# Optimization experiments

Hardware: AMD Instinct MI355X
Metric: run time of the kernel (lower is better)

## Reference

```python
import jax, jax.numpy as jnp
import numpy as np

EMB = 256
HID = 256
NH = 8
HD = HID // NH  # 32
EPS = 1e-5


def _wn(v, g):
    # torch weight_norm(dim=0): per-output-row normalization of v
    return g[:, None] * v / jnp.linalg.norm(v, axis=1, keepdims=True)


def _ln(x, gamma, beta):
    mu = jnp.mean(x, axis=-1, keepdims=True)
    var = jnp.mean((x - mu) ** 2, axis=-1, keepdims=True)
    return (x - mu) * jax.lax.rsqrt(var + EPS) * gamma + beta


def _rope(x):
    # x: [B', S, H, D]; torchtune-style rotary embedding, base 10000
    S, D = x.shape[1], x.shape[3]
    freqs = 1.0 / (10000.0 ** (jnp.arange(0, D, 2, dtype=jnp.float32) / D))  # [D/2]
    ang = jnp.arange(S, dtype=jnp.float32)[:, None] * freqs[None, :]          # [S, D/2]
    cos = jnp.cos(ang)[None, :, None, :]
    sin = jnp.sin(ang)[None, :, None, :]
    xr = x.reshape(*x.shape[:-1], D // 2, 2)
    x0, x1 = xr[..., 0], xr[..., 1]
    out = jnp.stack([x0 * cos - x1 * sin, x1 * cos + x0 * sin], axis=-1)
    return out.reshape(x.shape)


def setup_inputs() -> dict:
    key = jax.random.key(0)
    ks = jax.random.split(key, 12)
    s = lambda shp: 0.02
    return {
        "z": jax.random.normal(ks[0], (2, 32, 512, EMB), dtype=jnp.float32),
        "ln1_g": jnp.ones((EMB,), jnp.float32),
        "ln1_b": jnp.zeros((EMB,), jnp.float32),
        "proj_v": jax.random.normal(ks[1], (3 * HID, EMB), jnp.float32) * 0.02,
        "proj_g": jnp.ones((3 * HID,), jnp.float32),
        "proj_b": jnp.zeros((3 * HID,), jnp.float32),
        "ff_v": jax.random.normal(ks[2], (EMB, HID), jnp.float32) * 0.02,
        "ff_g": jnp.ones((EMB,), jnp.float32),
        "ff_b": jnp.zeros((EMB,), jnp.float32),
        "ln2_g": jnp.ones((EMB,), jnp.float32),
        "ln2_b": jnp.zeros((EMB,), jnp.float32),
        "w1_v": jax.random.normal(ks[3], (EMB, EMB), jnp.float32) * 0.02,
        "w1_g": jnp.ones((EMB,), jnp.float32),
        "w1_b": jnp.zeros((EMB,), jnp.float32),
        "w2_v": jax.random.normal(ks[4], (EMB, EMB), jnp.float32) * 0.02,
        "w2_g": jnp.ones((EMB,), jnp.float32),
        "w2_b": jnp.zeros((EMB,), jnp.float32),
    }


def reference(z, ln1_g, ln1_b, proj_v, proj_g, proj_b, ff_v, ff_g, ff_b,
              ln2_g, ln2_b, w1_v, w1_g, w1_b, w2_v, w2_g, w2_b):
    B, U, A, E = z.shape
    BU = B * U
    Wqkv = _wn(proj_v, proj_g)   # [3H, E]
    Wo = _wn(ff_v, ff_g)         # [E, H]
    # ---- RoPE attention block ----
    z_ = _ln(z, ln1_g, ln1_b).reshape(BU, A, E)
    qkv = z_ @ Wqkv.T + proj_b                       # [BU, A, 3H]
    qkv = qkv.reshape(BU, A, NH, 3 * HD)
    q, k, v = jnp.split(qkv, 3, axis=-1)             # each [BU, A, NH, HD]
    q = _rope(q)
    k = _rope(k)
    qh = q.transpose(0, 2, 1, 3)                     # [BU, NH, A, HD]
    kh = k.transpose(0, 2, 1, 3)
    vh = v.transpose(0, 2, 1, 3)
    scores = jnp.einsum('bhqd,bhkd->bhqk', qh, kh) / jnp.sqrt(jnp.float32(HD))
    attn = jax.nn.softmax(scores, axis=-1)
    out = jnp.einsum('bhqk,bhkd->bhqd', attn, vh)    # [BU, NH, A, HD]
    out = out.transpose(0, 2, 1, 3).reshape(BU, A, HID)
    out = out @ Wo.T + ff_b
    z = z + out.reshape(B, U, A, E)
    # ---- NormFF block ----
    W1 = _wn(w1_v, w1_g)
    W2 = _wn(w2_v, w2_g)
    h = _ln(z, ln2_g, ln2_b)
    h = jax.nn.gelu(h @ W1.T + w1_b, approximate=False)
    h = h @ W2.T + w2_b
    return z + h
```

## Files before the change

### kernel.cpp

```cpp
#include <hip/hip_runtime.h>
#include <cmath>

#define EMB 256
#define NHEAD 8
#define HD 32
#define A_LEN 512
#define TOK 32768

typedef __bf16 bf16_t;
typedef __bf16 bf16x8 __attribute__((ext_vector_type(8)));
typedef __bf16 bf16x4 __attribute__((ext_vector_type(4)));
typedef float floatx4 __attribute__((ext_vector_type(4)));

#define MFMA16(a, b, c) __builtin_amdgcn_mfma_f32_16x16x32_bf16((a), (b), (c), 0, 0, 0)

__global__ __launch_bounds__(64) void setup_kernel(
    const float* __restrict__ proj_v, const float* __restrict__ proj_g,
    const float* __restrict__ ff_v, const float* __restrict__ ff_g,
    const float* __restrict__ w1_v, const float* __restrict__ w1_g,
    const float* __restrict__ w2_v, const float* __restrict__ w2_g,
    bf16_t* __restrict__ Wall, float* __restrict__ ctab,
    float* __restrict__ stab) {
    int b = blockIdx.x;
    int lane = threadIdx.x;
    if (b < 1536) {
        const float* v; const float* g; int r;
        if (b < 768)       { v = proj_v; g = proj_g; r = b; }
        else if (b < 1024) { v = ff_v;   g = ff_g;   r = b - 768; }
        else if (b < 1280) { v = w1_v;   g = w1_g;   r = b - 1024; }
        else               { v = w2_v;   g = w2_g;   r = b - 1280; }
        const floatx4* vr = (const floatx4*)(v + (size_t)r * 256);
        floatx4 x = vr[lane];
        float ss = x[0] * x[0] + x[1] * x[1] + x[2] * x[2] + x[3] * x[3];
#pragma unroll
        for (int off = 32; off >= 1; off >>= 1) ss += __shfl_xor(ss, off);
        float sc = g[r] * rsqrtf(ss);
        bf16x4 o;
        o[0] = (bf16_t)(x[0] * sc); o[1] = (bf16_t)(x[1] * sc);
        o[2] = (bf16_t)(x[2] * sc); o[3] = (bf16_t)(x[3] * sc);
        ((bf16x4*)(Wall + (size_t)b * 256))[lane] = o;
    } else {
        int idx = (b - 1536) * 64 + lane;
        int a = idx >> 4, i = idx & 15;
        float freq = expf(-(float)(2 * i) * 0.2878231366242558f);
        float ang = (float)a * freq;
        ctab[idx] = cosf(ang);
        stab[idx] = sinf(ang);
    }
}

__global__ __launch_bounds__(256, 2) void qkv_kernel(
    const float* __restrict__ z, const float* __restrict__ ln_g,
    const float* __restrict__ ln_b, const bf16_t* __restrict__ W,
    const float* __restrict__ pb, const float* __restrict__ ctab,
    const float* __restrict__ stab, bf16_t* __restrict__ qbf,
    bf16_t* __restrict__ kbf, bf16_t* __restrict__ vtb) {
    __shared__ bf16_t xns[64 * 264];
    __shared__ bf16_t vls[256 * 72];
    int tid = threadIdx.x;
    int t0 = blockIdx.x * 64;

#pragma unroll
    for (int it = 0; it < 4; ++it) {
        int row = it * 16 + (tid >> 4);
        int sub = tid & 15;
        const floatx4* zr = (const floatx4*)(z + (size_t)(t0 + row) * 256 + sub * 16);
        floatx4 v0 = zr[0], v1 = zr[1], v2 = zr[2], v3 = zr[3];
        float vals[16];
        ((floatx4*)vals)[0] = v0; ((floatx4*)vals)[1] = v1;
        ((floatx4*)vals)[2] = v2; ((floatx4*)vals)[3] = v3;
        float s = 0.f, q2 = 0.f;
#pragma unroll
        for (int i = 0; i < 16; ++i) { s += vals[i]; q2 += vals[i] * vals[i]; }
#pragma unroll
        for (int off = 8; off >= 1; off >>= 1) {
            s += __shfl_xor(s, off);
            q2 += __shfl_xor(q2, off);
        }
        float mu = s * (1.f / 256.f);
        float inv = rsqrtf(q2 * (1.f / 256.f) - mu * mu + 1e-5f);
        int cb = sub * 16;
        bf16x8 o0, o1;
#pragma unroll
        for (int i = 0; i < 8; ++i)
            o0[i] = (bf16_t)((vals[i] - mu) * inv * ln_g[cb + i] + ln_b[cb + i]);
#pragma unroll
        for (int i = 0; i < 8; ++i)
            o1[i] = (bf16_t)((vals[8 + i] - mu) * inv * ln_g[cb + 8 + i] + ln_b[cb + 8 + i]);
        *(bf16x8*)&xns[row * 264 + cb] = o0;
        *(bf16x8*)&xns[row * 264 + cb + 8] = o1;
    }
    __syncthreads();

    int wv = tid >> 6, lane = tid & 63, quad = lane >> 4, lidx = lane & 15;

    bf16x8 afr[4][8];
#pragma unroll
    for (int mt = 0; mt < 4; ++mt)
#pragma unroll
        for (int kc = 0; kc < 8; ++kc)
            afr[mt][kc] = *(const bf16x8*)&xns[(mt * 16 + lidx) * 264 + kc * 32 + quad * 8];

#pragma unroll 1
    for (int nt = 0; nt < 12; ++nt) {
        int nbase = wv * 192 + nt * 16;
        int n = nbase + lidx;
        bf16x8 bfr[8];
#pragma unroll
        for (int kc = 0; kc < 8; ++kc)
            bfr[kc] = *(const bf16x8*)&W[(size_t)n * 256 + kc * 32 + quad * 8];
        floatx4 acc[4];
#pragma unroll
        for (int mt = 0; mt < 4; ++mt) acc[mt] = (floatx4){0.f, 0.f, 0.f, 0.f};
#pragma unroll
        for (int kc = 0; kc < 8; ++kc)
#pragma unroll
            for (int mt = 0; mt < 4; ++mt)
                acc[mt] = MFMA16(afr[mt][kc], bfr[kc], acc[mt]);

        float bias = pb[n];
        int htile = nbase / 96;
        int rem = nbase % 96;
        int sec = rem >> 5;
        int d = (rem & 31) + lidx;
#pragma unroll
        for (int mt = 0; mt < 4; ++mt) {
#pragma unroll
            for (int r = 0; r < 4; ++r) {
                int tok = t0 + mt * 16 + quad * 4 + r;
                int a = tok & 511;
                int bu = tok >> 9;
                float val = acc[mt][r] + bias;
                if (sec == 2) {
                    int a_loc = mt * 16 + quad * 4 + r;
                    vls[(htile * 32 + d) * 72 + a_loc] = (bf16_t)val;
                } else {
                    size_t addr = ((size_t)((bu * 8 + htile) * 512 + a)) * 32 + d;
                    float part = __shfl_xor(val, 1);
                    float cs = ctab[a * 16 + (d >> 1)];
                    float sn = stab[a * 16 + (d >> 1)];
                    float res = ((d & 1) == 0) ? (val * cs - part * sn)
                                               : (val * cs + part * sn);
                    if (sec == 0)
                        qbf[addr] = (bf16_t)(res * 0.17677669529663687f);
                    else
                        kbf[addr] = (bf16_t)res;
                }
            }
        }
    }
    __syncthreads();
    {
        int bu = t0 >> 9, a0 = t0 & 511;
        size_t gbase = ((size_t)(bu * 256 + tid)) * 512 + a0;
#pragma unroll
        for (int j = 0; j < 8; ++j)
            *(bf16x8*)&vtb[gbase + j * 8] = *(const bf16x8*)&vls[tid * 72 + j * 8];
    }
}

__global__ __launch_bounds__(512, 4) void attn_kernel(
    const bf16_t* __restrict__ qbf, const bf16_t* __restrict__ kbf,
    const bf16_t* __restrict__ vtb, bf16_t* __restrict__ ob) {
    __shared__ bf16_t Kls[512 * 32];
    __shared__ bf16_t Vt[32 * 512];
    __shared__ bf16_t Pls[8 * 16 * 64];
    int tid = threadIdx.x;
    int wv = tid >> 6, lane = tid & 63, quad = lane >> 4, lidx = lane & 15;
    int bh = blockIdx.x;
    int bu = bh >> 3, h = bh & 7;
    size_t hb = (size_t)bh * (A_LEN * HD);

#pragma unroll
    for (int i = 0; i < 4; ++i) {
        int c = tid + i * 512;
        int key = c >> 2, blk = c & 3;
        bf16x8 kv = *(const bf16x8*)&kbf[hb + (size_t)c * 8];
        *(bf16x8*)&Kls[key * 32 + ((blk ^ (key & 3)) << 3)] = kv;
        int vrow = c >> 6, vblk = c & 63;
        bf16x8 vv = *(const bf16x8*)&vtb[hb + (size_t)c * 8];
        *(bf16x8*)&Vt[vrow * 512 + ((vblk ^ (vrow & 7)) << 3)] = vv;
    }
    __syncthreads();

    int pbase = wv * (16 * 64);
    const floatx4 cm8 = (floatx4){-8.f, -8.f, -8.f, -8.f};
    const floatx4 zero4 = (floatx4){0.f, 0.f, 0.f, 0.f};

#pragma unroll 1
    for (int mt = 0; mt < 4; ++mt) {
        int q0 = wv * 64 + mt * 16;
        bf16x8 qfrag = *(const bf16x8*)&qbf[hb + (size_t)(q0 + lidx) * 32 + quad * 8];
        float l_[4] = {0.f, 0.f, 0.f, 0.f};
        floatx4 Oacc[2];
        Oacc[0] = zero4; Oacc[1] = zero4;

#pragma unroll 1
        for (int kc = 0; kc < 8; ++kc) {
            floatx4 sc[4];
#pragma unroll
            for (int t = 0; t < 4; ++t) {
                bf16x8 kf = *(const bf16x8*)&Kls[(kc * 64 + t * 16 + lidx) * 32 +
                                                 ((quad ^ (lidx & 3)) << 3)];
                sc[t] = MFMA16(qfrag, kf, cm8);
            }
            float p[4][4];
#pragma unroll
            for (int t = 0; t < 4; ++t)
#pragma unroll
                for (int r = 0; r < 4; ++r) p[t][r] = __expf(sc[t][r]);
#pragma unroll
            for (int t = 0; t < 4; ++t)
#pragma unroll
                for (int r = 0; r < 4; ++r) {
                    int row = quad * 4 + r;
                    int pc = (t * 16 + lidx) ^ ((row & 7) << 3);
                    Pls[pbase + row * 64 + pc] = (bf16_t)p[t][r];
                }
#pragma unroll
            for (int r = 0; r < 4; ++r) {
                float s = (p[0][r] + p[1][r]) + (p[2][r] + p[3][r]);
#pragma unroll
                for (int off = 8; off >= 1; off >>= 1) s += __shfl_xor(s, off);
                l_[r] += s;
            }
#pragma unroll
            for (int ks = 0; ks < 2; ++ks) {
                bf16x8 pf = *(const bf16x8*)&Pls[pbase + lidx * 64 +
                                                 (((ks * 4 + quad) ^ (lidx & 7)) << 3)];
#pragma unroll
                for (int nt = 0; nt < 2; ++nt) {
                    int vrow = nt * 16 + lidx;
                    bf16x8 vf = *(const bf16x8*)&Vt[vrow * 512 +
                        ((kc * 8 + ((ks * 4 + quad) ^ (lidx & 7))) << 3)];
                    Oacc[nt] = MFMA16(pf, vf, Oacc[nt]);
                }
            }
        }
#pragma unroll
        for (int nt = 0; nt < 2; ++nt)
#pragma unroll
            for (int r = 0; r < 4; ++r) {
                int tok = bu * 512 + q0 + quad * 4 + r;
                ob[(size_t)tok * 256 + h * 32 + nt * 16 + lidx] =
                    (bf16_t)(Oacc[nt][r] / l_[r]);
            }
    }
}

__global__ __launch_bounds__(256, 2) void tail_kernel(
    const bf16_t* __restrict__ X, const bf16_t* __restrict__ Wo,
    const float* __restrict__ obias, const float* __restrict__ zin,
    const float* __restrict__ ln_g, const float* __restrict__ ln_b,
    const bf16_t* __restrict__ W1, const float* __restrict__ b1,
    const bf16_t* __restrict__ W2, const float* __restrict__ b2,
    float* __restrict__ outp) {
    __shared__ bf16_t xns[64 * 264];
    __shared__ bf16_t hs[64 * 264];
    __shared__ float red[64 * 8];
    __shared__ float mi[64 * 2];
    int tid = threadIdx.x;
    int t0 = blockIdx.x * 64;
    int wv = tid >> 6, lane = tid & 63, quad = lane >> 4, lidx = lane & 15;

    bf16x8 afr[4][8];
#pragma unroll
    for (int mt = 0; mt < 4; ++mt)
#pragma unroll
        for (int kc = 0; kc < 8; ++kc)
            afr[mt][kc] = *(const bf16x8*)&X[(size_t)(t0 + mt * 16 + lidx) * 256 + kc * 32 + quad * 8];

    float r1[4][4][4];
#pragma unroll 1
    for (int nt = 0; nt < 4; ++nt) {
        int n = wv * 64 + nt * 16 + lidx;
        bf16x8 bfr[8];
#pragma unroll
        for (int kc = 0; kc < 8; ++kc)
            bfr[kc] = *(const bf16x8*)&Wo[(size_t)n * 256 + kc * 32 + quad * 8];
        floatx4 acc[4];
#pragma unroll
        for (int mt = 0; mt < 4; ++mt) acc[mt] = (floatx4){0.f, 0.f, 0.f, 0.f};
#pragma unroll
        for (int kc = 0; kc < 8; ++kc)
#pragma unroll
            for (int mt = 0; mt < 4; ++mt)
                acc[mt] = MFMA16(afr[mt][kc], bfr[kc], acc[mt]);
        float b = obias[n];
#pragma unroll
        for (int mt = 0; mt < 4; ++mt)
#pragma unroll
            for (int r = 0; r < 4; ++r) {
                size_t o = (size_t)(t0 + mt * 16 + quad * 4 + r) * 256 + n;
                r1[nt][mt][r] = zin[o] + acc[mt][r] + b;
            }
    }

#pragma unroll
    for (int mt = 0; mt < 4; ++mt)
#pragma unroll
        for (int r = 0; r < 4; ++r) {
            float s = 0.f, ss = 0.f;
#pragma unroll
            for (int nt = 0; nt < 4; ++nt) {
                float v = r1[nt][mt][r];
                s += v; ss += v * v;
            }
#pragma unroll
            for (int off = 8; off >= 1; off >>= 1) {
                s += __shfl_xor(s, off);
                ss += __shfl_xor(ss, off);
            }
            if (lidx == 0) {
                int row = mt * 16 + quad * 4 + r;
                red[row * 8 + wv * 2] = s;
                red[row * 8 + wv * 2 + 1] = ss;
            }
        }
    __syncthreads();
    if (tid < 64) {
        float s = 0.f, ss = 0.f;
#pragma unroll
        for (int w = 0; w < 4; ++w) {
            s += red[tid * 8 + w * 2];
            ss += red[tid * 8 + w * 2 + 1];
        }
        float mu = s * (1.f / 256.f);
        mi[tid * 2] = mu;
        mi[tid * 2 + 1] = rsqrtf(ss * (1.f / 256.f) - mu * mu + 1e-5f);
    }
    __syncthreads();

    float gv[4], bv[4];
#pragma unroll
    for (int nt = 0; nt < 4; ++nt) {
        int n = wv * 64 + nt * 16 + lidx;
        gv[nt] = ln_g[n]; bv[nt] = ln_b[n];
    }
#pragma unroll
    for (int mt = 0; mt < 4; ++mt)
#pragma unroll
        for (int r = 0; r < 4; ++r) {
            int row = mt * 16 + quad * 4 + r;
            float mu = mi[row * 2], inv = mi[row * 2 + 1];
#pragma unroll
            for (int nt = 0; nt < 4; ++nt) {
                int n = wv * 64 + nt * 16 + lidx;
                xns[row * 264 + n] = (bf16_t)((r1[nt][mt][r] - mu) * inv * gv[nt] + bv[nt]);
            }
        }
    __syncthreads();

#pragma unroll
    for (int mt = 0; mt < 4; ++mt)
#pragma unroll
        for (int kc = 0; kc < 8; ++kc)
            afr[mt][kc] = *(const bf16x8*)&xns[(mt * 16 + lidx) * 264 + kc * 32 + quad * 8];
#pragma unroll 1
    for (int nt = 0; nt < 4; ++nt) {
        int n = wv * 64 + nt * 16 + lidx;
        bf16x8 bfr[8];
#pragma unroll
        for (int kc = 0; kc < 8; ++kc)
            bfr[kc] = *(const bf16x8*)&W1[(size_t)n * 256 + kc * 32 + quad * 8];
        floatx4 acc[4];
#pragma unroll
        for (int mt = 0; mt < 4; ++mt) acc[mt] = (floatx4){0.f, 0.f, 0.f, 0.f};
#pragma unroll
        for (int kc = 0; kc < 8; ++kc)
#pragma unroll
            for (int mt = 0; mt < 4; ++mt)
                acc[mt] = MFMA16(afr[mt][kc], bfr[kc], acc[mt]);
        float b = b1[n];
#pragma unroll
        for (int mt = 0; mt < 4; ++mt)
#pragma unroll
            for (int r = 0; r < 4; ++r) {
                float x = acc[mt][r] + b;
                float gel = 0.5f * x * (1.f + erff(x * 0.7071067811865476f));
                hs[(mt * 16 + quad * 4 + r) * 264 + n] = (bf16_t)gel;
            }
    }
    __syncthreads();

#pragma unroll
    for (int mt = 0; mt < 4; ++mt)
#pragma unroll
        for (int kc = 0; kc < 8; ++kc)
            afr[mt][kc] = *(const bf16x8*)&hs[(mt * 16 + lidx) * 264 + kc * 32 + quad * 8];
#pragma unroll 1
    for (int nt = 0; nt < 4; ++nt) {
        int n = wv * 64 + nt * 16 + lidx;
        bf16x8 bfr[8];
#pragma unroll
        for (int kc = 0; kc < 8; ++kc)
            bfr[kc] = *(const bf16x8*)&W2[(size_t)n * 256 + kc * 32 + quad * 8];
        floatx4 acc[4];
#pragma unroll
        for (int mt = 0; mt < 4; ++mt) acc[mt] = (floatx4){0.f, 0.f, 0.f, 0.f};
#pragma unroll
        for (int kc = 0; kc < 8; ++kc)
#pragma unroll
            for (int mt = 0; mt < 4; ++mt)
                acc[mt] = MFMA16(afr[mt][kc], bfr[kc], acc[mt]);
        float b = b2[n];
#pragma unroll
        for (int mt = 0; mt < 4; ++mt)
#pragma unroll
            for (int r = 0; r < 4; ++r) {
                size_t o = (size_t)(t0 + mt * 16 + quad * 4 + r) * 256 + n;
                outp[o] = r1[nt][mt][r] + acc[mt][r] + b;
            }
    }
}

extern "C" void kernel_launch(void* const* d_in, const int* in_sizes, int n_in,
                              void* d_out, int out_size, void* d_ws, size_t ws_size,
                              hipStream_t stream) {
    const float* z      = (const float*)d_in[0];
    const float* ln1_g  = (const float*)d_in[1];
    const float* ln1_b  = (const float*)d_in[2];
    const float* proj_v = (const float*)d_in[3];
    const float* proj_g = (const float*)d_in[4];
    const float* proj_b = (const float*)d_in[5];
    const float* ff_v   = (const float*)d_in[6];
    const float* ff_g   = (const float*)d_in[7];
    const float* ff_b   = (const float*)d_in[8];
    const float* ln2_g  = (const float*)d_in[9];
    const float* ln2_b  = (const float*)d_in[10];
    const float* w1_v   = (const float*)d_in[11];
    const float* w1_g   = (const float*)d_in[12];
    const float* w1_b   = (const float*)d_in[13];
    const float* w2_v   = (const float*)d_in[14];
    const float* w2_g   = (const float*)d_in[15];
    const float* w2_b   = (const float*)d_in[16];
    float* out = (float*)d_out;

    char* p = (char*)d_ws;
    bf16_t* Wall = (bf16_t*)p; p += (size_t)1536 * 256 * 2;
    float* ctab  = (float*)p;  p += 8192 * 4;
    float* stab  = (float*)p;  p += 8192 * 4;
    bf16_t* qbf  = (bf16_t*)p; p += (size_t)TOK * 256 * 2;
    bf16_t* kbf  = (bf16_t*)p; p += (size_t)TOK * 256 * 2;
    bf16_t* vtb  = (bf16_t*)p; p += (size_t)TOK * 256 * 2;
    bf16_t* abuf = (bf16_t*)p; p += (size_t)TOK * 256 * 2;

    const bf16_t* Wqkv = Wall;
    const bf16_t* Wo   = Wall + (size_t)768 * 256;
    const bf16_t* W1   = Wall + (size_t)1024 * 256;
    const bf16_t* W2   = Wall + (size_t)1280 * 256;

    setup_kernel<<<1664, 64, 0, stream>>>(proj_v, proj_g, ff_v, ff_g,
                                          w1_v, w1_g, w2_v, w2_g,
                                          Wall, ctab, stab);
    qkv_kernel<<<TOK / 64, 256, 0, stream>>>(z, ln1_g, ln1_b, Wqkv, proj_b,
                                             ctab, stab, qbf, kbf, vtb);
    attn_kernel<<<64 * 8, 512, 0, stream>>>(qbf, kbf, vtb, abuf);
    tail_kernel<<<TOK / 64, 256, 0, stream>>>(abuf, Wo, ff_b, z, ln2_g, ln2_b,
                                              W1, w1_b, W2, w2_b, out);
}
```

Before: 289.0 us.

## Halve token tiles in QKV and tail kernels to raise occupancy

Shrinks the token tile in the QKV and tail GEMM kernels from 64 to 32 rows and raises launch bounds to 4 blocks per CU. The inner loops now stream A fragments from LDS per k-chunk instead of holding 32 register fragments, which cuts register and LDS pressure. The tail kernel reuses one LDS buffer across its stages and stages the final output through LDS so it can be written as coalesced float4 stores. Each block now reads every weight row for half as many tokens, so weight traffic per token doubles, and extra barriers are added.

```diff
diff --git a/kernel.cpp b/kernel.cpp
--- a/kernel.cpp
+++ b/kernel.cpp
@@ -49,19 +49,19 @@
     }
 }
 
-__global__ __launch_bounds__(256, 2) void qkv_kernel(
+__global__ __launch_bounds__(256, 4) void qkv_kernel(
     const float* __restrict__ z, const float* __restrict__ ln_g,
     const float* __restrict__ ln_b, const bf16_t* __restrict__ W,
     const float* __restrict__ pb, const float* __restrict__ ctab,
     const float* __restrict__ stab, bf16_t* __restrict__ qbf,
     bf16_t* __restrict__ kbf, bf16_t* __restrict__ vtb) {
-    __shared__ bf16_t xns[64 * 264];
-    __shared__ bf16_t vls[256 * 72];
+    __shared__ bf16_t xns[32 * 264];
+    __shared__ bf16_t vls[256 * 40];
     int tid = threadIdx.x;
-    int t0 = blockIdx.x * 64;
-
-#pragma unroll
-    for (int it = 0; it < 4; ++it) {
+    int t0 = blockIdx.x * 32;
+
+#pragma unroll
+    for (int it = 0; it < 2; ++it) {
         int row = it * 16 + (tid >> 4);
         int sub = tid & 15;
         const floatx4* zr = (const floatx4*)(z + (size_t)(t0 + row) * 256 + sub * 16);
@@ -94,68 +94,69 @@
 
     int wv = tid >> 6, lane = tid & 63, quad = lane >> 4, lidx = lane & 15;
 
-    bf16x8 afr[4][8];
-#pragma unroll
-    for (int mt = 0; mt < 4; ++mt)
-#pragma unroll
-        for (int kc = 0; kc < 8; ++kc)
-            afr[mt][kc] = *(const bf16x8*)&xns[(mt * 16 + lidx) * 264 + kc * 32 + quad * 8];
-
 #pragma unroll 1
-    for (int nt = 0; nt < 12; ++nt) {
-        int nbase = wv * 192 + nt * 16;
-        int n = nbase + lidx;
-        bf16x8 bfr[8];
-#pragma unroll
-        for (int kc = 0; kc < 8; ++kc)
-            bfr[kc] = *(const bf16x8*)&W[(size_t)n * 256 + kc * 32 + quad * 8];
-        floatx4 acc[4];
-#pragma unroll
-        for (int mt = 0; mt < 4; ++mt) acc[mt] = (floatx4){0.f, 0.f, 0.f, 0.f};
-#pragma unroll
-        for (int kc = 0; kc < 8; ++kc)
-#pragma unroll
-            for (int mt = 0; mt < 4; ++mt)
-                acc[mt] = MFMA16(afr[mt][kc], bfr[kc], acc[mt]);
-
-        float bias = pb[n];
-        int htile = nbase / 96;
-        int rem = nbase % 96;
-        int sec = rem >> 5;
-        int d = (rem & 31) + lidx;
-#pragma unroll
-        for (int mt = 0; mt < 4; ++mt) {
-#pragma unroll
-            for (int r = 0; r < 4; ++r) {
-                int tok = t0 + mt * 16 + quad * 4 + r;
-                int a = tok & 511;
-                int bu = tok >> 9;
-                float val = acc[mt][r] + bias;
-                if (sec == 2) {
+    for (int g = 0; g < 3; ++g) {
+        floatx4 acc[4][2];
+#pragma unroll
+        for (int i = 0; i < 4; ++i) {
+            acc[i][0] = (floatx4){0.f, 0.f, 0.f, 0.f};
+            acc[i][1] = (floatx4){0.f, 0.f, 0.f, 0.f};
+        }
+#pragma unroll 2
+        for (int kc = 0; kc < 8; ++kc) {
+            bf16x8 a0 = *(const bf16x8*)&xns[lidx * 264 + kc * 32 + quad * 8];
+            bf16x8 a1 = *(const bf16x8*)&xns[(16 + lidx) * 264 + kc * 32 + quad * 8];
+#pragma unroll
+            for (int ntl = 0; ntl < 4; ++ntl) {
+                int n = wv * 192 + (g * 4 + ntl) * 16 + lidx;
+                bf16x8 bfr = *(const bf16x8*)&W[(size_t)n * 256 + kc * 32 + quad * 8];
+                acc[ntl][0] = MFMA16(a0, bfr, acc[ntl][0]);
+                acc[ntl][1] = MFMA16(a1, bfr, acc[ntl][1]);
+            }
+        }
+#pragma unroll
+        for (int ntl = 0; ntl < 4; ++ntl) {
+            int nbase = wv * 192 + (g * 4 + ntl) * 16;
+            int n = nbase + lidx;
+            float bias = pb[n];
+            int htile = nbase / 96;
+            int rem = nbase % 96;
+            int sec = rem >> 5;
+            int d = (rem & 31) + lidx;
+#pragma unroll
+            for (int mt = 0; mt < 2; ++mt) {
+#pragma unroll
+                for (int r = 0; r < 4; ++r) {
                     int a_loc = mt * 16 + quad * 4 + r;
-                    vls[(htile * 32 + d) * 72 + a_loc] = (bf16_t)val;
-                } else {
-                    size_t addr = ((size_t)((bu * 8 + htile) * 512 + a)) * 32 + d;
-                    float part = __shfl_xor(val, 1);
-                    float cs = ctab[a * 16 + (d >> 1)];
-                    float sn = stab[a * 16 + (d >> 1)];
-                    float res = ((d & 1) == 0) ? (val * cs - part * sn)
-                                               : (val * cs + part * sn);
-                    if (sec == 0)
-                        qbf[addr] = (bf16_t)(res * 0.17677669529663687f);
-                    else
-                        kbf[addr] = (bf16_t)res;
-                }
-            }
-        }
-    }
-    __syncthreads();
-    {
-        int bu = t0 >> 9, a0 = t0 & 511;
-        size_t gbase = ((size_t)(bu * 256 + tid)) * 512 + a0;
-#pragma unroll
-        for (int j = 0; j < 8; ++j)
-            *(bf16x8*)&vtb[gbase + j * 8] = *(const bf16x8*)&vls[tid * 72 + j * 8];
+                    int tok = t0 + a_loc;
+                    int a = tok & 511;
+                    int bu = tok >> 9;
+                    float val = acc[ntl][mt][r] + bias;
+                    if (sec == 2) {
+                        vls[(htile * 32 + d) * 40 + a_loc] = (bf16_t)val;
+                    } else {
+                        size_t addr = ((size_t)((bu * 8 + htile) * 512 + a)) * 32 + d;
+                        float part = __shfl_xor(val, 1);
+                        float cs = ctab[a * 16 + (d >> 1)];
+                        float sn = stab[a * 16 + (d >> 1)];
+                        float res = ((d & 1) == 0) ? (val * cs - part * sn)
+                                                   : (val * cs + part * sn);
+                        if (sec == 0)
+                            qbf[addr] = (bf16_t)(res * 0.17677669529663687f);
+                        else
+                            kbf[addr] = (bf16_t)res;
+                    }
+                }
+            }
+        }
+    }
+    __syncthreads();
+    {
+        int bu = t0 >> 9, ac0 = t0 & 511;
+        size_t gbase = ((size_t)(bu * 256 + tid)) * 512 + ac0;
+#pragma unroll
+        for (int j = 0; j < 4; ++j)
+            *(bf16x8*)&vtb[gbase + j * 8] = *(const bf16x8*)&vls[tid * 40 + j * 8];
     }
 }
 
@@ -248,56 +249,66 @@
     }
 }
 
-__global__ __launch_bounds__(256, 2) void tail_kernel(
+__global__ __launch_bounds__(256, 4) void tail_kernel(
     const bf16_t* __restrict__ X, const bf16_t* __restrict__ Wo,
     const float* __restrict__ obias, const float* __restrict__ zin,
     const float* __restrict__ ln_g, const float* __restrict__ ln_b,
     const bf16_t* __restrict__ W1, const float* __restrict__ b1,
     const bf16_t* __restrict__ W2, const float* __restrict__ b2,
     float* __restrict__ outp) {
-    __shared__ bf16_t xns[64 * 264];
-    __shared__ bf16_t hs[64 * 264];
-    __shared__ float red[64 * 8];
-    __shared__ float mi[64 * 2];
+    __shared__ float fbuf[32 * 264];
+    __shared__ float red[32 * 8];
+    __shared__ float mi[32 * 2];
+    bf16_t* xbuf = (bf16_t*)fbuf;
     int tid = threadIdx.x;
-    int t0 = blockIdx.x * 64;
+    int t0 = blockIdx.x * 32;
     int wv = tid >> 6, lane = tid & 63, quad = lane >> 4, lidx = lane & 15;
 
-    bf16x8 afr[4][8];
-#pragma unroll
-    for (int mt = 0; mt < 4; ++mt)
-#pragma unroll
-        for (int kc = 0; kc < 8; ++kc)
-            afr[mt][kc] = *(const bf16x8*)&X[(size_t)(t0 + mt * 16 + lidx) * 256 + kc * 32 + quad * 8];
-
-    float r1[4][4][4];
-#pragma unroll 1
-    for (int nt = 0; nt < 4; ++nt) {
-        int n = wv * 64 + nt * 16 + lidx;
-        bf16x8 bfr[8];
-#pragma unroll
-        for (int kc = 0; kc < 8; ++kc)
-            bfr[kc] = *(const bf16x8*)&Wo[(size_t)n * 256 + kc * 32 + quad * 8];
-        floatx4 acc[4];
-#pragma unroll
-        for (int mt = 0; mt < 4; ++mt) acc[mt] = (floatx4){0.f, 0.f, 0.f, 0.f};
-#pragma unroll
-        for (int kc = 0; kc < 8; ++kc)
-#pragma unroll
-            for (int mt = 0; mt < 4; ++mt)
-                acc[mt] = MFMA16(afr[mt][kc], bfr[kc], acc[mt]);
-        float b = obias[n];
-#pragma unroll
-        for (int mt = 0; mt < 4; ++mt)
-#pragma unroll
-            for (int r = 0; r < 4; ++r) {
-                size_t o = (size_t)(t0 + mt * 16 + quad * 4 + r) * 256 + n;
-                r1[nt][mt][r] = zin[o] + acc[mt][r] + b;
-            }
-    }
-
-#pragma unroll
-    for (int mt = 0; mt < 4; ++mt)
+    {
+        int row = tid >> 3;
+        int c0 = (tid & 7) * 32;
+        const bf16x8* src = (const bf16x8*)&X[(size_t)(t0 + row) * 256 + c0];
+        bf16x8* dst = (bf16x8*)&xbuf[row * 264 + c0];
+        dst[0] = src[0]; dst[1] = src[1]; dst[2] = src[2]; dst[3] = src[3];
+    }
+    __syncthreads();
+
+    float r1[4][2][4];
+    {
+        floatx4 acc[4][2];
+#pragma unroll
+        for (int i = 0; i < 4; ++i) {
+            acc[i][0] = (floatx4){0.f, 0.f, 0.f, 0.f};
+            acc[i][1] = (floatx4){0.f, 0.f, 0.f, 0.f};
+        }
+#pragma unroll 2
+        for (int kc = 0; kc < 8; ++kc) {
+            bf16x8 a0 = *(const bf16x8*)&xbuf[lidx * 264 + kc * 32 + quad * 8];
+            bf16x8 a1 = *(const bf16x8*)&xbuf[(16 + lidx) * 264 + kc * 32 + quad * 8];
+#pragma unroll
+            for (int nt = 0; nt < 4; ++nt) {
+                int n = wv * 64 + nt * 16 + lidx;
+                bf16x8 bfr = *(const bf16x8*)&Wo[(size_t)n * 256 + kc * 32 + quad * 8];
+                acc[nt][0] = MFMA16(a0, bfr, acc[nt][0]);
+                acc[nt][1] = MFMA16(a1, bfr, acc[nt][1]);
+            }
+        }
+#pragma unroll
+        for (int nt = 0; nt < 4; ++nt) {
+            int n = wv * 64 + nt * 16 + lidx;
+            float b = obias[n];
+#pragma unroll
+            for (int mt = 0; mt < 2; ++mt)
+#pragma unroll
+                for (int r = 0; r < 4; ++r) {
+                    size_t o = (size_t)(t0 + mt * 16 + quad * 4 + r) * 256 + n;
+                    r1[nt][mt][r] = zin[o] + acc[nt][mt][r] + b;
+                }
+        }
+    }
+
+#pragma unroll
+    for (int mt = 0; mt < 2; ++mt)
 #pragma unroll
         for (int r = 0; r < 4; ++r) {
             float s = 0.f, ss = 0.f;
@@ -318,7 +329,7 @@
             }
         }
     __syncthreads();
-    if (tid < 64) {
+    if (tid < 32) {
         float s = 0.f, ss = 0.f;
 #pragma unroll
         for (int w = 0; w < 4; ++w) {
@@ -331,86 +342,106 @@
     }
     __syncthreads();
 
-    float gv[4], bv[4];
-#pragma unroll
-    for (int nt = 0; nt < 4; ++nt) {
-        int n = wv * 64 + nt * 16 + lidx;
-        gv[nt] = ln_g[n]; bv[nt] = ln_b[n];
-    }
-#pragma unroll
-    for (int mt = 0; mt < 4; ++mt)
-#pragma unroll
-        for (int r = 0; r < 4; ++r) {
-            int row = mt * 16 + quad * 4 + r;
-            float mu = mi[row * 2], inv = mi[row * 2 + 1];
+    {
+        float gv[4], bv[4];
+#pragma unroll
+        for (int nt = 0; nt < 4; ++nt) {
+            int n = wv * 64 + nt * 16 + lidx;
+            gv[nt] = ln_g[n]; bv[nt] = ln_b[n];
+        }
+#pragma unroll
+        for (int mt = 0; mt < 2; ++mt)
+#pragma unroll
+            for (int r = 0; r < 4; ++r) {
+                int row = mt * 16 + quad * 4 + r;
+                float mu = mi[row * 2], inv = mi[row * 2 + 1];
+#pragma unroll
+                for (int nt = 0; nt < 4; ++nt) {
+                    int n = wv * 64 + nt * 16 + lidx;
+                    xbuf[row * 264 + n] =
+                        (bf16_t)((r1[nt][mt][r] - mu) * inv * gv[nt] + bv[nt]);
+                }
+            }
+    }
+    __syncthreads();
+
+    {
+        floatx4 acc[4][2];
+#pragma unroll
+        for (int i = 0; i < 4; ++i) {
+            acc[i][0] = (floatx4){0.f, 0.f, 0.f, 0.f};
+            acc[i][1] = (floatx4){0.f, 0.f, 0.f, 0.f};
+        }
+#pragma unroll 2
+        for (int kc = 0; kc < 8; ++kc) {
+            bf16x8 a0 = *(const bf16x8*)&xbuf[lidx * 264 + kc * 32 + quad * 8];
+            bf16x8 a1 = *(const bf16x8*)&xbuf[(16 + lidx) * 264 + kc * 32 + quad * 8];
 #pragma unroll
             for (int nt = 0; nt < 4; ++nt) {
                 int n = wv * 64 + nt * 16 + lidx;
-                xns[row * 264 + n] = (bf16_t)((r1[nt][mt][r] - mu) * inv * gv[nt] + bv[nt]);
-            }
-        }
-    __syncthreads();
-
-#pragma unroll
-    for (int mt = 0; mt < 4; ++mt)
-#pragma unroll
-        for (int kc = 0; kc < 8; ++kc)
-            afr[mt][kc] = *(const bf16x8*)&xns[(mt * 16 + lidx) * 264 + kc * 32 + quad * 8];
-#pragma unroll 1
-    for (int nt = 0; nt < 4; ++nt) {
-        int n = wv * 64 + nt * 16 + lidx;
-        bf16x8 bfr[8];
-#pragma unroll
-        for (int kc = 0; kc < 8; ++kc)
-            bfr[kc] = *(const bf16x8*)&W1[(size_t)n * 256 + kc * 32 + quad * 8];
-        floatx4 acc[4];
-#pragma unroll
-        for (int mt = 0; mt < 4; ++mt) acc[mt] = (floatx4){0.f, 0.f, 0.f, 0.f};
-#pragma unroll
-        for (int kc = 0; kc < 8; ++kc)
-#pragma unroll
-            for (int mt = 0; mt < 4; ++mt)
-                acc[mt] = MFMA16(afr[mt][kc], bfr[kc], acc[mt]);
-        float b = b1[n];
-#pragma unroll
-        for (int mt = 0; mt < 4; ++mt)
-#pragma unroll
-            for (int r = 0; r < 4; ++r) {
-                float x = acc[mt][r] + b;
-                float gel = 0.5f * x * (1.f + erff(x * 0.7071067811865476f));
-                hs[(mt * 16 + quad * 4 + r) * 264 + n] = (bf16_t)gel;
-            }
-    }
-    __syncthreads();
-
-#pragma unroll
-    for (int mt = 0; mt < 4; ++mt)
-#pragma unroll
-        for (int kc = 0; kc < 8; ++kc)
-            afr[mt][kc] = *(const bf16x8*)&hs[(mt * 16 + lidx) * 264 + kc * 32 + quad * 8];
-#pragma unroll 1
-    for (int nt = 0; nt < 4; ++nt) {
-        int n = wv * 64 + nt * 16 + lidx;
-        bf16x8 bfr[8];
-#pragma unroll
-        for (int kc = 0; kc < 8; ++kc)
-            bfr[kc] = *(const bf16x8*)&W2[(size_t)n * 256 + kc * 32 + quad * 8];
-        floatx4 acc[4];
-#pragma unroll
-        for (int mt = 0; mt < 4; ++mt) acc[mt] = (floatx4){0.f, 0.f, 0.f, 0.f};
-#pragma unroll
-        for (int kc = 0; kc < 8; ++kc)
-#pragma unroll
-            for (int mt = 0; mt < 4; ++mt)
-                acc[mt] = MFMA16(afr[mt][kc], bfr[kc], acc[mt]);
-        float b = b2[n];
-#pragma unroll
-        for (int mt = 0; mt < 4; ++mt)
-#pragma unroll
-            for (int r = 0; r < 4; ++r) {
-                size_t o = (size_t)(t0 + mt * 16 + quad * 4 + r) * 256 + n;
-                outp[o] = r1[nt][mt][r] + acc[mt][r] + b;
-            }
+                bf16x8 bfr = *(const bf16x8*)&W1[(size_t)n * 256 + kc * 32 + quad * 8];
+                acc[nt][0] = MFMA16(a0, bfr, acc[nt][0]);
+                acc[nt][1] = MFMA16(a1, bfr, acc[nt][1]);
+            }
+        }
+        __syncthreads();
+#pragma unroll
+        for (int nt = 0; nt < 4; ++nt) {
+            int n = wv * 64 + nt * 16 + lidx;
+            float b = b1[n];
+#pragma unroll
+            for (int mt = 0; mt < 2; ++mt)
+#pragma unroll
+                for (int r = 0; r < 4; ++r) {
+                    float x = acc[nt][mt][r] + b;
+                    float gel = 0.5f * x * (1.f + erff(x * 0.7071067811865476f));
+                    xbuf[(mt * 16 + quad * 4 + r) * 264 + n] = (bf16_t)gel;
+                }
+        }
+    }
+    __syncthreads();
+
+    {
+        floatx4 acc[4][2];
+#pragma unroll
+        for (int i = 0; i < 4; ++i) {
+            acc[i][0] = (floatx4){0.f, 0.f, 0.f, 0.f};
+            acc[i][1] = (floatx4){0.f, 0.f, 0.f, 0.f};
+        }
+#pragma unroll 2
+        for (int kc = 0; kc < 8; ++kc) {
+            bf16x8 a0 = *(const bf16x8*)&xbuf[lidx * 264 + kc * 32 + quad * 8];
+            bf16x8 a1 = *(const bf16x8*)&xbuf[(16 + lidx) * 264 + kc * 32 + quad * 8];
+#pragma unroll
+            for (int nt = 0; nt < 4; ++nt) {
+                int n = wv * 64 + nt * 16 + lidx;
+                bf16x8 bfr = *(const bf16x8*)&W2[(size_t)n * 256 + kc * 32 + quad * 8];
+                acc[nt][0] = MFMA16(a0, bfr, acc[nt][0]);
+                acc[nt][1] = MFMA16(a1, bfr, acc[nt][1]);
+            }
+        }
+        __syncthreads();
+#pragma unroll
+        for (int nt = 0; nt < 4; ++nt) {
+            int n = wv * 64 + nt * 16 + lidx;
+            float b = b2[n];
+#pragma unroll
+            for (int mt = 0; mt < 2; ++mt)
+#pragma unroll
+                for (int r = 0; r < 4; ++r)
+                    fbuf[(mt * 16 + quad * 4 + r) * 264 + n] =
+                        r1[nt][mt][r] + acc[nt][mt][r] + b;
+        }
+    }
+    __syncthreads();
+
+#pragma unroll
+    for (int i = 0; i < 8; ++i) {
+        int fid = i * 256 + tid;
+        int row = fid >> 6;
+        int c4 = (fid & 63) * 4;
+        *(floatx4*)&outp[(size_t)(t0 + row) * 256 + c4] =
+            *(const floatx4*)&fbuf[row * 264 + c4];
     }
 }
 
@@ -453,9 +484,9 @@
     setup_kernel<<<1664, 64, 0, stream>>>(proj_v, proj_g, ff_v, ff_g,
                                           w1_v, w1_g, w2_v, w2_g,
                                           Wall, ctab, stab);
-    qkv_kernel<<<TOK / 64, 256, 0, stream>>>(z, ln1_g, ln1_b, Wqkv, proj_b,
+    qkv_kernel<<<TOK / 32, 256, 0, stream>>>(z, ln1_g, ln1_b, Wqkv, proj_b,
                                              ctab, stab, qbf, kbf, vtb);
     attn_kernel<<<64 * 8, 512, 0, stream>>>(qbf, kbf, vtb, abuf);
-    tail_kernel<<<TOK / 64, 256, 0, stream>>>(abuf, Wo, ff_b, z, ln2_g, ln2_b,
+    tail_kernel<<<TOK / 32, 256, 0, stream>>>(abuf, Wo, ff_b, z, ln2_g, ln2_b,
                                               W1, w1_b, W2, w2_b, out);
 }
```

Measured after the change: 294.6 us. Within noise of the previous version (+2.0%).
